# Kernel tuning notes

Hardware: AMD Instinct MI355X
Metric: run time of the kernel (lower is better)

Reference implementation:

```python
import math
import jax, jax.numpy as jnp
import numpy as np

B, S, D = 8, 1024, 1024
H, DK = 16, 64
NUM_BUCKETS, MAX_DIST = 32, 128
LN_EPS = 1e-6


def _relative_position_bucket(relative_position, num_buckets=NUM_BUCKETS, max_distance=MAX_DIST):
    # bidirectional (encoder) variant of T5 bucketing
    nb = num_buckets // 2
    rel_buckets = (relative_position > 0).astype(jnp.int32) * nb
    rp = jnp.abs(relative_position)
    max_exact = nb // 2
    is_small = rp < max_exact
    rp_large = max_exact + (
        jnp.log(jnp.maximum(rp, 1).astype(jnp.float32) / max_exact)
        / math.log(max_distance / max_exact)
        * (nb - max_exact)
    ).astype(jnp.int32)
    rp_large = jnp.minimum(rp_large, nb - 1)
    return rel_buckets + jnp.where(is_small, rp, rp_large)


def compute_bias(rel_bias, q_len, k_len):
    ctx = jnp.arange(q_len)[:, None]
    mem = jnp.arange(k_len)[None, :]
    buckets = _relative_position_bucket(mem - ctx)        # [q,k]
    values = rel_bias[buckets]                             # [q,k,H]
    return jnp.transpose(values, (2, 0, 1))[None]          # [1,H,q,k]


def switch_layer_norm(x, w, eps=LN_EPS):
    # T5-style: no mean subtraction, no bias
    var = jnp.mean(jnp.square(x.astype(jnp.float32)), axis=-1, keepdims=True)
    return w * (x * jax.lax.rsqrt(var + eps)).astype(x.dtype)


def setup_inputs() -> dict:
    key = jax.random.key(0)
    ks = jax.random.split(key, 6)
    scale = 1.0 / math.sqrt(D)
    return {
        "hidden_states": jax.random.normal(ks[0], (B, S, D), jnp.float32),
        "ln_weight": jnp.ones((D,), jnp.float32),
        "wq": jax.random.normal(ks[1], (D, H * DK), jnp.float32) * scale,
        "wk": jax.random.normal(ks[2], (D, H * DK), jnp.float32) * scale,
        "wv": jax.random.normal(ks[3], (D, H * DK), jnp.float32) * scale,
        "wo": jax.random.normal(ks[4], (H * DK, D), jnp.float32) * scale,
        "rel_bias": jax.random.normal(ks[5], (NUM_BUCKETS, H), jnp.float32),
    }


def reference(hidden_states, ln_weight, wq, wk, wv, wo, rel_bias):
    b, s, d = hidden_states.shape
    normed = switch_layer_norm(hidden_states, ln_weight)
    # projections -> [B,H,S,DK]; T5 applies NO 1/sqrt(dk) scaling
    q = (normed @ wq).reshape(b, s, H, DK).transpose(0, 2, 1, 3)
    k = (normed @ wk).reshape(b, s, H, DK).transpose(0, 2, 1, 3)
    v = (normed @ wv).reshape(b, s, H, DK).transpose(0, 2, 1, 3)
    scores = jnp.einsum("bhqd,bhkd->bhqk", q, k)
    scores = scores + compute_bias(rel_bias, s, s)
    attn = jax.nn.softmax(scores, axis=-1)
    ctx = jnp.einsum("bhqk,bhkd->bhqd", attn, v)
    ctx = ctx.transpose(0, 2, 1, 3).reshape(b, s, H * DK)
    attn_out = ctx @ wo
    return hidden_states + attn_out  # residual of SwitchLayerSelfAttention (dropout=0)
```

## Files before the change

kernel.cpp:

```cpp
#include <hip/hip_runtime.h>

typedef unsigned short u16;
typedef unsigned int u32;
typedef unsigned long long u64;
typedef __attribute__((ext_vector_type(8))) short bf16x8;
typedef __attribute__((ext_vector_type(4))) float f32x4;

__device__ __forceinline__ float bf2f(u16 u) {
  union { u32 i; float f; } c; c.i = ((u32)u) << 16; return c.f;
}
__device__ __forceinline__ u16 f2bf(float f) {
  union { float f; u32 i; } c; c.f = f;
  u32 i = c.i;
  return (u16)((i + 0x7fffu + ((i >> 16) & 1u)) >> 16);
}
__device__ __forceinline__ u32 pkbf(float a, float b) {
  union { float f; u32 i; } ca, cb; ca.f = a; cb.f = b;
  return __builtin_amdgcn_perm(cb.i + 0x8000u, ca.i + 0x8000u, 0x07060302u);
}
__device__ __forceinline__ void async16(const void* g, void* l) {
  __builtin_amdgcn_global_load_lds((const __attribute__((address_space(1))) void*)g,
                                   (__attribute__((address_space(3))) void*)l, 16, 0, 0);
}

__global__ __launch_bounds__(256) void detect_kernel(const u32* __restrict__ X,
                                                     int* __restrict__ flag) {
  __shared__ int part[4];
  const int tid = threadIdx.x, lane = tid & 63, wave = tid >> 6;
  int votes = 0;
  for (int i = tid; i < 4096; i += 256) {
    const u32 u = X[i];
    union { u32 i; float f; } c; c.i = u;
    const float a = fabsf(c.f);
    if (u == 0u || (a > 1e-6f && a < 1e6f)) votes++;
  }
  #pragma unroll
  for (int off = 32; off >= 1; off >>= 1) votes += __shfl_xor(votes, off);
  if (lane == 0) part[wave] = votes;
  __syncthreads();
  if (tid == 0) {
    const int tot = part[0] + part[1] + part[2] + part[3];
    *flag = (tot >= 2048) ? 0 : 1;
  }
}

__global__ __launch_bounds__(256) void prep_kernel(
    const void* __restrict__ W0, const void* __restrict__ W1, const void* __restrict__ W2,
    const void* __restrict__ W3, u16* __restrict__ T0, u16* __restrict__ T1,
    u16* __restrict__ T2, u16* __restrict__ T3, const void* __restrict__ rel_bias,
    float* __restrict__ Tb, const int* __restrict__ flagp) {
  const int f32m = (*flagp == 0);
  const int z = blockIdx.z;
  if (z == 4) {
    const int flat = blockIdx.y * 16 + blockIdx.x;
    const int idx = flat * 256 + threadIdx.x;
    if (idx >= 16 * 2047) return;
    const int h = idx / 2047;
    const int d = idx % 2047 - 1023;
    const int rb = (d > 0) ? 16 : 0;
    const int rp = d < 0 ? -d : d;
    int val;
    if (rp < 8) {
      val = rp;
    } else {
      float t = (logf((float)rp * 0.125f) / 2.772588722239781f) * 8.0f;
      val = 8 + (int)t;
      if (val > 15) val = 15;
    }
    const int bi = (rb + val) * 16 + h;
    Tb[idx] = f32m ? ((const float*)rel_bias)[bi] : bf2f(((const u16*)rel_bias)[bi]);
    return;
  }
  const void* W = (z == 0) ? W0 : (z == 1) ? W1 : (z == 2) ? W2 : W3;
  u16* WT = (z == 0) ? T0 : (z == 1) ? T1 : (z == 2) ? T2 : T3;
  __shared__ u16 t[64][65];
  const int tid = threadIdx.x;
  const int tx = tid & 63, ty = tid >> 6;
  const int n0 = blockIdx.x * 64, k0 = blockIdx.y * 64;
  #pragma unroll
  for (int r = ty; r < 64; r += 4) {
    const size_t idx = (size_t)(k0 + r) * 1024 + n0 + tx;
    t[r][tx] = f32m ? f2bf(((const float*)W)[idx]) : ((const u16*)W)[idx];
  }
  __syncthreads();
  #pragma unroll
  for (int r = ty; r < 64; r += 4) WT[(size_t)(n0 + r) * 1024 + k0 + tx] = t[tx][r];
}

__global__ __launch_bounds__(256) void rmsnorm_kernel(const void* __restrict__ X,
                                                      const void* __restrict__ W,
                                                      u16* __restrict__ Out,
                                                      const int* __restrict__ flagp) {
  const int f32m = (*flagp == 0);
  __shared__ float part[4];
  const int tid = threadIdx.x, lane = tid & 63, wave = tid >> 6;
  const size_t row = blockIdx.x;
  const int c = tid * 4;
  float x0, x1, x2, x3, w0f, w1f, w2f, w3f;
  if (f32m) {
    const float4 xx = *(const float4*)((const float*)X + row * 1024 + c);
    x0 = xx.x; x1 = xx.y; x2 = xx.z; x3 = xx.w;
    const float4 ww = *(const float4*)((const float*)W + c);
    w0f = ww.x; w1f = ww.y; w2f = ww.z; w3f = ww.w;
  } else {
    const u32* px = (const u32*)((const u16*)X + row * 1024 + c);
    const u32 a0 = px[0], a1 = px[1];
    x0 = bf2f((u16)a0); x1 = bf2f((u16)(a0 >> 16));
    x2 = bf2f((u16)a1); x3 = bf2f((u16)(a1 >> 16));
    const u32* pw = (const u32*)((const u16*)W + c);
    const u32 b0 = pw[0], b1 = pw[1];
    w0f = bf2f((u16)b0); w1f = bf2f((u16)(b0 >> 16));
    w2f = bf2f((u16)b1); w3f = bf2f((u16)(b1 >> 16));
  }
  float ss = x0 * x0 + x1 * x1 + x2 * x2 + x3 * x3;
  #pragma unroll
  for (int off = 32; off >= 1; off >>= 1) ss += __shfl_xor(ss, off);
  if (lane == 0) part[wave] = ss;
  __syncthreads();
  const float tot = part[0] + part[1] + part[2] + part[3];
  const float scale = rsqrtf(tot * (1.0f / 1024.0f) + 1e-6f);
  const u16 o0 = f2bf(x0 * scale * w0f);
  const u16 o1 = f2bf(x1 * scale * w1f);
  const u16 o2 = f2bf(x2 * scale * w2f);
  const u16 o3 = f2bf(x3 * scale * w3f);
  u32* po = (u32*)(Out + row * 1024 + c);
  po[0] = (u32)o0 | ((u32)o1 << 16);
  po[1] = (u32)o2 | ((u32)o3 << 16);
}

template <bool SWAP>
__device__ __forceinline__ void gemm_core(const u16* __restrict__ A, const u16* __restrict__ BT,
                                          u16* As, u16* Bs, f32x4 (&acc)[4][4],
                                          int m0, int n0, int K, int lane, int wave) {
  const int srow = lane >> 2, scol = (lane & 3) * 8;
  const int wm = (wave >> 1) * 64, wn = (wave & 1) * 64;
  for (int kt = 0; kt < K; kt += 32) {
    __syncthreads();
    #pragma unroll
    for (int i = 0; i < 2; ++i) {
      const int c = wave * 2 + i;
      async16(A + (size_t)(m0 + c * 16 + srow) * K + kt + scol, As + c * 512);
      async16(BT + (size_t)(n0 + c * 16 + srow) * K + kt + scol, Bs + c * 512);
    }
    __syncthreads();
    bf16x8 af[4], bfr[4];
    #pragma unroll
    for (int mt = 0; mt < 4; ++mt)
      af[mt] = *(const bf16x8*)(As + (wm + mt * 16 + (lane & 15)) * 32 + (lane >> 4) * 8);
    #pragma unroll
    for (int nt = 0; nt < 4; ++nt)
      bfr[nt] = *(const bf16x8*)(Bs + (wn + nt * 16 + (lane & 15)) * 32 + (lane >> 4) * 8);
    #pragma unroll
    for (int mt = 0; mt < 4; ++mt)
      #pragma unroll
      for (int nt = 0; nt < 4; ++nt) {
        if (SWAP)
          acc[mt][nt] = __builtin_amdgcn_mfma_f32_16x16x32_bf16(bfr[nt], af[mt], acc[mt][nt], 0, 0, 0);
        else
          acc[mt][nt] = __builtin_amdgcn_mfma_f32_16x16x32_bf16(af[mt], bfr[nt], acc[mt][nt], 0, 0, 0);
      }
  }
}

__global__ __launch_bounds__(256) void qkv_gemm_kernel(
    const u16* __restrict__ A, const u16* __restrict__ WT,
    u16* __restrict__ Qo, u16* __restrict__ Ko, u16* __restrict__ Vo, int K) {
  __shared__ __align__(16) u16 As[128 * 32];
  __shared__ __align__(16) u16 Bs[128 * 32];
  const int tid = threadIdx.x, lane = tid & 63, wave = tid >> 6;
  const int id = blockIdx.x;
  const int xcd = id & 7;
  const int t = id >> 3;
  const int nb = t % 24;
  const int mhi = t / 24;
  const int m0 = (mhi * 8 + xcd) * 128;
  const int n0 = nb * 128;
  const int z = nb >> 3;

  f32x4 acc[4][4];
  const f32x4 zero = {0.f, 0.f, 0.f, 0.f};
  #pragma unroll
  for (int i = 0; i < 4; ++i)
    #pragma unroll
    for (int j = 0; j < 4; ++j) acc[i][j] = zero;

  const int wm = (wave >> 1) * 64, wn = (wave & 1) * 64;
  if (z == 2) {
    gemm_core<false>(A, WT, As, Bs, acc, m0, n0, K, lane, wave);
    #pragma unroll
    for (int mt = 0; mt < 4; ++mt) {
      const int mrow0 = m0 + wm + mt * 16 + (lane >> 4) * 4;
      const int b = mrow0 >> 10;
      const int s0 = mrow0 & 1023;
      #pragma unroll
      for (int nt = 0; nt < 4; ++nt) {
        const int n = (n0 + wn + nt * 16 + (lane & 15)) & 1023;
        const int hh = n >> 6, dk = n & 63;
        const u64 pk = (u64)f2bf(acc[mt][nt][0]) | ((u64)f2bf(acc[mt][nt][1]) << 16) |
                       ((u64)f2bf(acc[mt][nt][2]) << 32) | ((u64)f2bf(acc[mt][nt][3]) << 48);
        *(u64*)(Vo + (((size_t)(b * 16 + hh)) * 64 + dk) * 1024 + s0) = pk;
      }
    }
  } else {
    gemm_core<true>(A, WT, As, Bs, acc, m0, n0, K, lane, wave);
    u16* Out = (z == 0) ? Qo : Ko;
    #pragma unroll
    for (int mt = 0; mt < 4; ++mt) {
      const int s = m0 + wm + mt * 16 + (lane & 15);
      const int b = s >> 10, ss = s & 1023;
      #pragma unroll
      for (int nt = 0; nt < 4; ++nt) {
        const int n = (n0 + wn + nt * 16 + (lane >> 4) * 4) & 1023;
        const int hh = n >> 6, dk = n & 63;
        const u64 pk = (u64)f2bf(acc[mt][nt][0]) | ((u64)f2bf(acc[mt][nt][1]) << 16) |
                       ((u64)f2bf(acc[mt][nt][2]) << 32) | ((u64)f2bf(acc[mt][nt][3]) << 48);
        *(u64*)(Out + (((size_t)(b * 16 + hh)) * 1024 + ss) * 64 + dk) = pk;
      }
    }
  }
}

__global__ __launch_bounds__(256) void out_gemm_kernel(
    const u16* __restrict__ A, const u16* __restrict__ BT, const void* __restrict__ Res,
    void* __restrict__ Out, int N, int K, const int* __restrict__ flagp) {
  const int f32m = (*flagp == 0);
  __shared__ __align__(16) u16 As[128 * 32];
  __shared__ __align__(16) u16 Bs[128 * 32];
  const int tid = threadIdx.x, lane = tid & 63, wave = tid >> 6;
  const int id = blockIdx.x;
  const int xcd = id & 7;
  const int t = id >> 3;
  const int nb = t & 7;
  const int mhi = t >> 3;
  const int m0 = (mhi * 8 + xcd) * 128;
  const int n0 = nb * 128;

  f32x4 acc[4][4];
  const f32x4 zero = {0.f, 0.f, 0.f, 0.f};
  #pragma unroll
  for (int i = 0; i < 4; ++i)
    #pragma unroll
    for (int j = 0; j < 4; ++j) acc[i][j] = zero;

  gemm_core<true>(A, BT, As, Bs, acc, m0, n0, K, lane, wave);

  const int wm = (wave >> 1) * 64, wn = (wave & 1) * 64;
  #pragma unroll
  for (int mt = 0; mt < 4; ++mt) {
    const int s = m0 + wm + mt * 16 + (lane & 15);
    #pragma unroll
    for (int nt = 0; nt < 4; ++nt) {
      const int n = n0 + wn + nt * 16 + (lane >> 4) * 4;
      const size_t idx = (size_t)s * N + n;
      if (f32m) {
        const float4 rr = *(const float4*)((const float*)Res + idx);
        float4 oo;
        oo.x = rr.x + acc[mt][nt][0]; oo.y = rr.y + acc[mt][nt][1];
        oo.z = rr.z + acc[mt][nt][2]; oo.w = rr.w + acc[mt][nt][3];
        *(float4*)((float*)Out + idx) = oo;
      } else {
        const u64 rr = *(const u64*)((const u16*)Res + idx);
        const u64 pk =
            (u64)f2bf(bf2f((u16)rr) + acc[mt][nt][0]) |
            ((u64)f2bf(bf2f((u16)(rr >> 16)) + acc[mt][nt][1]) << 16) |
            ((u64)f2bf(bf2f((u16)(rr >> 32)) + acc[mt][nt][2]) << 32) |
            ((u64)f2bf(bf2f((u16)(rr >> 48)) + acc[mt][nt][3]) << 48);
        *(u64*)((u16*)Out + idx) = pk;
      }
    }
  }
}

__global__ __launch_bounds__(256, 3) void attn_kernel(
    const u16* __restrict__ Q, const u16* __restrict__ K, const u16* __restrict__ VT,
    const float* __restrict__ Tb, u16* __restrict__ ctx) {
  __shared__ __align__(16) u16 Ks[2][4096];
  __shared__ __align__(16) u16 Vs[2][4096];
  __shared__ __align__(16) u16 Ps[4][2048];
  __shared__ __align__(16) float Tbs[1152];

  const int tid = threadIdx.x, lane = tid & 63, w = tid >> 6;
  const int c = lane & 15, quad = lane >> 4;
  const int id = blockIdx.x;
  const int bh = id & 127, qc = id >> 7;
  const int b = bh >> 4, h = bh & 15;
  const int q0 = qc * 128;
  const int qw = q0 + w * 32;
  const u16* Kg = K + (size_t)bh * 1024 * 64;
  const u16* Vg = VT + (size_t)bh * 64 * 1024;
  const float* Th = Tb + h * 2047;
  u16* PsW = &Ps[w][0];

  #pragma unroll
  for (int i = tid; i < 1152; i += 256) Tbs[i] = Th[896 - q0 + i];

  bf16x8 qf[2][2];
  {
    const u16* Qg = Q + ((size_t)bh * 1024 + qw) * 64;
    #pragma unroll
    for (int nt = 0; nt < 2; ++nt)
      #pragma unroll
      for (int half = 0; half < 2; ++half)
        qf[nt][half] = *(const bf16x8*)(Qg + (size_t)(nt * 16 + c) * 64 + half * 32 + quad * 8);
  }

  f32x4 oacc[4][2];
  const f32x4 zero = {0.f, 0.f, 0.f, 0.f};
  #pragma unroll
  for (int i = 0; i < 4; ++i)
    #pragma unroll
    for (int j = 0; j < 2; ++j) oacc[i][j] = zero;
  float rsum[2] = {0.f, 0.f};

  {
    const int k0 = 0;
    #pragma unroll
    for (int i = 0; i < 2; ++i) {
      async16(Kg + (size_t)(k0 + w * 16 + c) * 64 + i * 32 + quad * 8, &Ks[0][(w * 2 + i) * 512]);
      async16(Vg + (size_t)(w * 16 + c) * 1024 + k0 + i * 32 + quad * 8, &Vs[0][(w * 2 + i) * 512]);
    }
  }

  #pragma unroll 1
  for (int kt = 0; kt < 16; ++kt) {
    const int cur = kt & 1;
    __asm__ volatile("s_waitcnt vmcnt(0)" ::: "memory");
    __syncthreads();
    if (kt < 15) {
      const int k1 = (kt + 1) * 64;
      #pragma unroll
      for (int i = 0; i < 2; ++i) {
        async16(Kg + (size_t)(k1 + w * 16 + c) * 64 + i * 32 + quad * 8,
                &Ks[1 - cur][(w * 2 + i) * 512]);
        async16(Vg + (size_t)(w * 16 + c) * 1024 + k1 + i * 32 + quad * 8,
                &Vs[1 - cur][(w * 2 + i) * 512]);
      }
    }
    const int k0 = kt * 64;
    f32x4 sc[4][2];
    const int jb = k0 + quad * 4 - c + 127 - 32 * w;
    #pragma unroll
    for (int mt = 0; mt < 4; ++mt)
      #pragma unroll
      for (int nt = 0; nt < 2; ++nt) {
        const float* tp = Tbs + jb + mt * 16 - nt * 16;
        sc[mt][nt][0] = tp[0]; sc[mt][nt][1] = tp[1]; sc[mt][nt][2] = tp[2]; sc[mt][nt][3] = tp[3];
      }
    const u16* Kc = &Ks[cur][0];
    #pragma unroll
    for (int mt = 0; mt < 4; ++mt) {
      const bf16x8 kf0 = *(const bf16x8*)(Kc + (mt * 2 + 0) * 512 + lane * 8);
      const bf16x8 kf1 = *(const bf16x8*)(Kc + (mt * 2 + 1) * 512 + lane * 8);
      #pragma unroll
      for (int nt = 0; nt < 2; ++nt) {
        sc[mt][nt] = __builtin_amdgcn_mfma_f32_16x16x32_bf16(kf0, qf[nt][0], sc[mt][nt], 0, 0, 0);
        sc[mt][nt] = __builtin_amdgcn_mfma_f32_16x16x32_bf16(kf1, qf[nt][1], sc[mt][nt], 0, 0, 0);
      }
    }
    #pragma unroll
    for (int mt = 0; mt < 4; ++mt)
      #pragma unroll
      for (int nt = 0; nt < 2; ++nt) {
        const float p0 = __expf(sc[mt][nt][0]), p1 = __expf(sc[mt][nt][1]);
        const float p2 = __expf(sc[mt][nt][2]), p3 = __expf(sc[mt][nt][3]);
        rsum[nt] += (p0 + p1) + (p2 + p3);
        const u32 lo = pkbf(p0, p1), hi = pkbf(p2, p3);
        const u64 pk = (u64)lo | ((u64)hi << 32);
        const int ch = (mt * 2 + (quad >> 1)) ^ (c & 7);
        *(u64*)(PsW + (nt * 16 + c) * 64 + ch * 8 + (quad & 1) * 4) = pk;
      }
    __asm__ volatile("s_waitcnt lgkmcnt(0)" ::: "memory");
    const u16* Vc = &Vs[cur][0];
    bf16x8 pf[2][2];
    #pragma unroll
    for (int nt = 0; nt < 2; ++nt)
      #pragma unroll
      for (int kk = 0; kk < 2; ++kk) {
        const int ch = (kk * 4 + quad) ^ (c & 7);
        pf[nt][kk] = *(const bf16x8*)(PsW + (nt * 16 + c) * 64 + ch * 8);
      }
    #pragma unroll
    for (int dt = 0; dt < 4; ++dt) {
      const bf16x8 vf0 = *(const bf16x8*)(Vc + (dt * 2 + 0) * 512 + lane * 8);
      const bf16x8 vf1 = *(const bf16x8*)(Vc + (dt * 2 + 1) * 512 + lane * 8);
      #pragma unroll
      for (int nt = 0; nt < 2; ++nt) {
        oacc[dt][nt] = __builtin_amdgcn_mfma_f32_16x16x32_bf16(vf0, pf[nt][0], oacc[dt][nt], 0, 0, 0);
        oacc[dt][nt] = __builtin_amdgcn_mfma_f32_16x16x32_bf16(vf1, pf[nt][1], oacc[dt][nt], 0, 0, 0);
      }
    }
  }

  #pragma unroll
  for (int nt = 0; nt < 2; ++nt) {
    rsum[nt] += __shfl_xor(rsum[nt], 16);
    rsum[nt] += __shfl_xor(rsum[nt], 32);
  }

  #pragma unroll
  for (int nt = 0; nt < 2; ++nt) {
    const float inv = 1.0f / rsum[nt];
    const int q = qw + nt * 16 + c;
    #pragma unroll
    for (int dt = 0; dt < 4; ++dt) {
      const u64 pk = (u64)f2bf(oacc[dt][nt][0] * inv) | ((u64)f2bf(oacc[dt][nt][1] * inv) << 16) |
                     ((u64)f2bf(oacc[dt][nt][2] * inv) << 32) | ((u64)f2bf(oacc[dt][nt][3] * inv) << 48);
      *(u64*)(ctx + (((size_t)b * 1024 + q) * 16 + h) * 64 + dt * 16 + quad * 4) = pk;
    }
  }
}

extern "C" void kernel_launch(void* const* d_in, const int* in_sizes, int n_in,
                              void* d_out, int out_size, void* d_ws, size_t ws_size,
                              hipStream_t stream) {
  const void* hidden = d_in[0];
  const void* lnw = d_in[1];
  const void* wq = d_in[2];
  const void* wk = d_in[3];
  const void* wv = d_in[4];
  const void* wo = d_in[5];
  const void* relb = d_in[6];
  char* ws = (char*)d_ws;

  u16* normed = (u16*)(ws);
  u16* Qb = (u16*)(ws + ((size_t)16 << 20));
  u16* Kb = (u16*)(ws + ((size_t)32 << 20));
  u16* VTb = (u16*)(ws + ((size_t)48 << 20));
  u16* wtq = (u16*)(ws + ((size_t)64 << 20));
  u16* wtk = (u16*)(ws + ((size_t)64 << 20) + (2 << 20));
  u16* wtv = (u16*)(ws + ((size_t)64 << 20) + (4 << 20));
  u16* wto = (u16*)(ws + ((size_t)64 << 20) + (6 << 20));
  float* Tb = (float*)(ws + ((size_t)64 << 20) + (8 << 20));
  int* flag = (int*)(ws + ((size_t)64 << 20) + (9 << 20));

  dim3 b256(256);
  detect_kernel<<<dim3(1), b256, 0, stream>>>((const u32*)hidden, flag);
  prep_kernel<<<dim3(16, 16, 5), b256, 0, stream>>>(wq, wk, wv, wo, wtq, wtk, wtv, wto,
                                                    relb, Tb, flag);
  rmsnorm_kernel<<<dim3(8192), b256, 0, stream>>>(hidden, lnw, normed, flag);
  qkv_gemm_kernel<<<dim3(1536), b256, 0, stream>>>(normed, wtq, Qb, Kb, VTb, 1024);
  attn_kernel<<<dim3(1024), b256, 0, stream>>>(Qb, Kb, VTb, Tb, normed);
  out_gemm_kernel<<<dim3(512), b256, 0, stream>>>(normed, wto, hidden, d_out, 1024, 1024, flag);
}
```

Measured before the change: 281.9 us.

## Rewrite QKV GEMM with 256x128 tiles and triple-buffered async LDS pipeline

Replaces the QKV projection GEMM with a 512-thread kernel that computes 256x128 output tiles, using a 64-wide K step and a three-stage LDS ring filled by direct global-to-LDS async loads with XOR swizzling. Loads for the next stage are issued in two halves between MFMA phases, with explicit waitcnt/barrier sequencing and setprio around MFMA bursts. The aim is to hide global memory latency and halve the number of times A is reloaded per output column. In exchange it uses about 144KB of LDS per block and hand-tuned sync, which limits occupancy and risks hazards if the counts are wrong.

```diff
diff --git a/kernel.cpp b/kernel.cpp
--- a/kernel.cpp
+++ b/kernel.cpp
@@ -162,18 +162,125 @@
   }
 }
 
-__global__ __launch_bounds__(256) void qkv_gemm_kernel(
+
+template <int S0>
+__device__ __forceinline__ void stage3(u16* lds, const u16* __restrict__ A,
+                                       const u16* __restrict__ B, int m0, int n0,
+                                       int kt, int w, int lane) {
+  const int ko8 = ((lane & 7) ^ ((lane >> 3) & 7)) * 8;
+  const int rl = lane >> 3;
+  #pragma unroll
+  for (int s = S0; s < S0 + 3; ++s) {
+    const int cw = s * 8 + w;
+    const int r = cw * 8 + rl;
+    u16* ldst = lds + cw * 512;
+    if (s < 4)
+      async16(A + (size_t)(m0 + r) * 1024 + kt + ko8, ldst);
+    else
+      async16(B + (size_t)(n0 + r - 256) * 1024 + kt + ko8, ldst);
+  }
+}
+
+template <bool SWAP>
+__device__ __forceinline__ void gemm256_core(const u16* __restrict__ A,
+                                             const u16* __restrict__ WT,
+                                             u16 (*buf)[24576], f32x4 (&acc)[4][4],
+                                             int m0, int n0, int lane, int w) {
+  const int wr = w >> 1, wc = w & 1;
+  const int l15 = lane & 15;
+  const int ko0 = (((lane >> 4) + 0) ^ (lane & 7)) * 8;
+  const int ko1 = (((lane >> 4) + 4) ^ (lane & 7)) * 8;
+  const int arow = (wr * 64 + l15) * 64;
+  const int brow = 16384 + (wc * 64 + l15) * 64;
+
+  stage3<0>(buf[0], A, WT, m0, n0, 0, w, lane);
+  stage3<3>(buf[0], A, WT, m0, n0, 0, w, lane);
+  stage3<0>(buf[1], A, WT, m0, n0, 64, w, lane);
+  stage3<3>(buf[1], A, WT, m0, n0, 64, w, lane);
+  __asm__ volatile("s_waitcnt vmcnt(6)" ::: "memory");
+  __builtin_amdgcn_s_barrier();
+  __asm__ volatile("" ::: "memory");
+
+  int sl = 0, sn = 2;
+  #pragma unroll 1
+  for (int t = 0; t < 16; ++t) {
+    const u16* bc = buf[sl];
+    u16* bn = buf[sn];
+    const int kt2 = (t + 2) * 64;
+    bf16x8 af[4][2], bfr[2][2];
+    #pragma unroll
+    for (int i = 0; i < 4; ++i) {
+      af[i][0] = *(const bf16x8*)(bc + arow + i * 1024 + ko0);
+      af[i][1] = *(const bf16x8*)(bc + arow + i * 1024 + ko1);
+    }
+    #pragma unroll
+    for (int j = 0; j < 2; ++j) {
+      bfr[j][0] = *(const bf16x8*)(bc + brow + j * 1024 + ko0);
+      bfr[j][1] = *(const bf16x8*)(bc + brow + j * 1024 + ko1);
+    }
+    if (t < 14) stage3<0>(bn, A, WT, m0, n0, kt2, w, lane);
+    __builtin_amdgcn_s_barrier();
+    __asm__ volatile("s_waitcnt lgkmcnt(0)" ::: "memory");
+    __builtin_amdgcn_s_setprio(1);
+    #pragma unroll
+    for (int i = 0; i < 4; ++i)
+      #pragma unroll
+      for (int j = 0; j < 2; ++j) {
+        if (SWAP) {
+          acc[i][j] = __builtin_amdgcn_mfma_f32_16x16x32_bf16(bfr[j][0], af[i][0], acc[i][j], 0, 0, 0);
+          acc[i][j] = __builtin_amdgcn_mfma_f32_16x16x32_bf16(bfr[j][1], af[i][1], acc[i][j], 0, 0, 0);
+        } else {
+          acc[i][j] = __builtin_amdgcn_mfma_f32_16x16x32_bf16(af[i][0], bfr[j][0], acc[i][j], 0, 0, 0);
+          acc[i][j] = __builtin_amdgcn_mfma_f32_16x16x32_bf16(af[i][1], bfr[j][1], acc[i][j], 0, 0, 0);
+        }
+      }
+    __builtin_amdgcn_s_setprio(0);
+    __builtin_amdgcn_s_barrier();
+    __asm__ volatile("" ::: "memory");
+    #pragma unroll
+    for (int j = 0; j < 2; ++j) {
+      bfr[j][0] = *(const bf16x8*)(bc + brow + (j + 2) * 1024 + ko0);
+      bfr[j][1] = *(const bf16x8*)(bc + brow + (j + 2) * 1024 + ko1);
+    }
+    if (t < 14) stage3<3>(bn, A, WT, m0, n0, kt2, w, lane);
+    __builtin_amdgcn_s_barrier();
+    __asm__ volatile("s_waitcnt lgkmcnt(0)" ::: "memory");
+    __builtin_amdgcn_s_setprio(1);
+    #pragma unroll
+    for (int i = 0; i < 4; ++i)
+      #pragma unroll
+      for (int j = 0; j < 2; ++j) {
+        if (SWAP) {
+          acc[i][j + 2] = __builtin_amdgcn_mfma_f32_16x16x32_bf16(bfr[j][0], af[i][0], acc[i][j + 2], 0, 0, 0);
+          acc[i][j + 2] = __builtin_amdgcn_mfma_f32_16x16x32_bf16(bfr[j][1], af[i][1], acc[i][j + 2], 0, 0, 0);
+        } else {
+          acc[i][j + 2] = __builtin_amdgcn_mfma_f32_16x16x32_bf16(af[i][0], bfr[j][0], acc[i][j + 2], 0, 0, 0);
+          acc[i][j + 2] = __builtin_amdgcn_mfma_f32_16x16x32_bf16(af[i][1], bfr[j][1], acc[i][j + 2], 0, 0, 0);
+        }
+      }
+    __builtin_amdgcn_s_setprio(0);
+    if (t < 14)
+      __asm__ volatile("s_waitcnt vmcnt(6)" ::: "memory");
+    else
+      __asm__ volatile("s_waitcnt vmcnt(0)" ::: "memory");
+    __builtin_amdgcn_s_barrier();
+    __asm__ volatile("" ::: "memory");
+    sl = (sl == 2) ? 0 : sl + 1;
+    sn = (sn == 2) ? 0 : sn + 1;
+  }
+}
+
+__global__ __launch_bounds__(512, 2) void qkv_gemm256_kernel(
     const u16* __restrict__ A, const u16* __restrict__ WT,
-    u16* __restrict__ Qo, u16* __restrict__ Ko, u16* __restrict__ Vo, int K) {
-  __shared__ __align__(16) u16 As[128 * 32];
-  __shared__ __align__(16) u16 Bs[128 * 32];
-  const int tid = threadIdx.x, lane = tid & 63, wave = tid >> 6;
+    u16* __restrict__ Qo, u16* __restrict__ Ko, u16* __restrict__ VTo) {
+  __shared__ __align__(16) u16 buf[3][24576];
+  const int tid = threadIdx.x, lane = tid & 63, w = tid >> 6;
   const int id = blockIdx.x;
   const int xcd = id & 7;
-  const int t = id >> 3;
-  const int nb = t % 24;
-  const int mhi = t / 24;
-  const int m0 = (mhi * 8 + xcd) * 128;
+  const int t0 = id >> 3;
+  const int nb = t0 % 24;
+  const int mhi = t0 / 24;
+  const int m0 = (mhi * 8 + xcd) * 256;
   const int n0 = nb * 128;
   const int z = nb >> 3;
 
@@ -184,36 +291,38 @@
     #pragma unroll
     for (int j = 0; j < 4; ++j) acc[i][j] = zero;
 
-  const int wm = (wave >> 1) * 64, wn = (wave & 1) * 64;
+  const int wr = w >> 1, wc = w & 1;
+  const int cq = lane & 15, quad = lane >> 4;
+  const int nbase = (n0 & 1023) + wc * 64;
+
   if (z == 2) {
-    gemm_core<false>(A, WT, As, Bs, acc, m0, n0, K, lane, wave);
-    #pragma unroll
-    for (int mt = 0; mt < 4; ++mt) {
-      const int mrow0 = m0 + wm + mt * 16 + (lane >> 4) * 4;
-      const int b = mrow0 >> 10;
-      const int s0 = mrow0 & 1023;
-      #pragma unroll
-      for (int nt = 0; nt < 4; ++nt) {
-        const int n = (n0 + wn + nt * 16 + (lane & 15)) & 1023;
+    gemm256_core<false>(A, WT, buf, acc, m0, n0, lane, w);
+    #pragma unroll
+    for (int i = 0; i < 4; ++i) {
+      const int s = m0 + wr * 64 + i * 16 + quad * 4;
+      const int b = s >> 10, s0 = s & 1023;
+      #pragma unroll
+      for (int j = 0; j < 4; ++j) {
+        const int n = nbase + j * 16 + cq;
         const int hh = n >> 6, dk = n & 63;
-        const u64 pk = (u64)f2bf(acc[mt][nt][0]) | ((u64)f2bf(acc[mt][nt][1]) << 16) |
-                       ((u64)f2bf(acc[mt][nt][2]) << 32) | ((u64)f2bf(acc[mt][nt][3]) << 48);
-        *(u64*)(Vo + (((size_t)(b * 16 + hh)) * 64 + dk) * 1024 + s0) = pk;
+        const u64 pk = (u64)f2bf(acc[i][j][0]) | ((u64)f2bf(acc[i][j][1]) << 16) |
+                       ((u64)f2bf(acc[i][j][2]) << 32) | ((u64)f2bf(acc[i][j][3]) << 48);
+        *(u64*)(VTo + (((size_t)(b * 16 + hh)) * 64 + dk) * 1024 + s0) = pk;
       }
     }
   } else {
-    gemm_core<true>(A, WT, As, Bs, acc, m0, n0, K, lane, wave);
+    gemm256_core<true>(A, WT, buf, acc, m0, n0, lane, w);
     u16* Out = (z == 0) ? Qo : Ko;
     #pragma unroll
-    for (int mt = 0; mt < 4; ++mt) {
-      const int s = m0 + wm + mt * 16 + (lane & 15);
+    for (int i = 0; i < 4; ++i) {
+      const int s = m0 + wr * 64 + i * 16 + cq;
       const int b = s >> 10, ss = s & 1023;
       #pragma unroll
-      for (int nt = 0; nt < 4; ++nt) {
-        const int n = (n0 + wn + nt * 16 + (lane >> 4) * 4) & 1023;
+      for (int j = 0; j < 4; ++j) {
+        const int n = nbase + j * 16 + quad * 4;
         const int hh = n >> 6, dk = n & 63;
-        const u64 pk = (u64)f2bf(acc[mt][nt][0]) | ((u64)f2bf(acc[mt][nt][1]) << 16) |
-                       ((u64)f2bf(acc[mt][nt][2]) << 32) | ((u64)f2bf(acc[mt][nt][3]) << 48);
+        const u64 pk = (u64)f2bf(acc[i][j][0]) | ((u64)f2bf(acc[i][j][1]) << 16) |
+                       ((u64)f2bf(acc[i][j][2]) << 32) | ((u64)f2bf(acc[i][j][3]) << 48);
         *(u64*)(Out + (((size_t)(b * 16 + hh)) * 1024 + ss) * 64 + dk) = pk;
       }
     }
@@ -438,7 +547,7 @@
   prep_kernel<<<dim3(16, 16, 5), b256, 0, stream>>>(wq, wk, wv, wo, wtq, wtk, wtv, wto,
                                                     relb, Tb, flag);
   rmsnorm_kernel<<<dim3(8192), b256, 0, stream>>>(hidden, lnw, normed, flag);
-  qkv_gemm_kernel<<<dim3(1536), b256, 0, stream>>>(normed, wtq, Qb, Kb, VTb, 1024);
+  qkv_gemm256_kernel<<<dim3(768), dim3(512), 0, stream>>>(normed, wtq, Qb, Kb, VTb);
   attn_kernel<<<dim3(1024), b256, 0, stream>>>(Qb, Kb, VTb, Tb, normed);
   out_gemm_kernel<<<dim3(512), b256, 0, stream>>>(normed, wto, hidden, d_out, 1024, 1024, flag);
 }
```

Result: no change. 278.9 us (-1.1%).
